# Optimization experiments

Measured on AMD Instinct MI355X. Metric: run time of the kernel, lower is better.

Reference implementation:

```python
import jax, jax.numpy as jnp
import numpy as np

DT = 0.042


def setup_inputs() -> dict:
    key = jax.random.key(0)
    ks = jax.random.split(key, 6)
    B, L, I, H = 64, 1024, 128, 512
    x = jax.random.normal(ks[0], (B, L, I), dtype=jnp.float32)
    x2h = jax.random.uniform(ks[1], (I, H), dtype=jnp.float32)  # rand * input_scaling (=1.0)
    h2h = jax.random.normal(ks[2], (H, H), dtype=jnp.float32) * (0.99 / (H ** 0.5))  # spectral-norm scaled
    bias = jax.random.uniform(ks[3], (H,), dtype=jnp.float32) * 2.0 - 1.0
    gamma = jax.random.uniform(ks[4], (H,), dtype=jnp.float32) + 2.0   # in [2, 3)
    epsilon = jax.random.uniform(ks[5], (H,), dtype=jnp.float32) + 4.0  # in [4, 5)
    return {"x": x, "x2h": x2h, "h2h": h2h, "bias": bias, "gamma": gamma, "epsilon": epsilon}


def reference(x, x2h, h2h, bias, gamma, epsilon):
    # x: (B, L, I). Precompute input projection for all timesteps in one GEMM.
    B, L, I = x.shape
    H = h2h.shape[0]
    u = jnp.einsum('bli,ih->blh', x, x2h) + bias  # (B, L, H)

    def step(carry, u_t):
        hy, hz = carry
        hz = hz + DT * (jnp.tanh(u_t + hy @ h2h) - gamma * hy - epsilon * hz)
        hy = hy + DT * hz
        return (hy, hz), hy

    init = (jnp.zeros((B, H), dtype=x.dtype), jnp.zeros((B, H), dtype=x.dtype))
    (hy_final, _), ys = jax.lax.scan(step, init, jnp.swapaxes(u, 0, 1))  # ys: (L, B, H)
    all_states = jnp.swapaxes(ys, 0, 1)  # (B, L, H)
    return all_states, hy_final
```

## Files before the change

### kernel.cpp

```cpp
#include <hip/hip_runtime.h>

#define DT 0.042f
constexpr int B = 64, L = 1024, I = 128, H = 512;

constexpr int NG = 32;
constexpr int NS = 8;
constexpr int GB = B / NG;
constexpr int SC = H / NS;

__global__ __launch_bounds__(256) void k_ugemm(const float* __restrict__ x,
                                               const float* __restrict__ w,
                                               const float* __restrict__ bias,
                                               float* __restrict__ u) {
    __shared__ __align__(16) float a_s[64][132];
    __shared__ __align__(16) float b_s[128][68];
    const int tx = threadIdx.x & 15;
    const int ty = threadIdx.x >> 4;
    const int row0 = blockIdx.x * 64;
    const int col0 = blockIdx.y * 64;

    for (int i = threadIdx.x; i < 64 * 32; i += 256) {
        int r = i >> 5, c4 = (i & 31) << 2;
        *(float4*)&a_s[r][c4] = *(const float4*)(x + (size_t)(row0 + r) * I + c4);
    }
    for (int i = threadIdx.x; i < 128 * 16; i += 256) {
        int k = i >> 4, c4 = (i & 15) << 2;
        *(float4*)&b_s[k][c4] = *(const float4*)(w + (size_t)k * H + col0 + c4);
    }
    __syncthreads();

    float acc[4][4] = {};
    for (int k = 0; k < I; k += 4) {
        float a4[4][4], b4[4][4];
        #pragma unroll
        for (int i = 0; i < 4; ++i) *(float4*)a4[i] = *(const float4*)&a_s[ty * 4 + i][k];
        #pragma unroll
        for (int kk = 0; kk < 4; ++kk) *(float4*)b4[kk] = *(const float4*)&b_s[k + kk][tx * 4];
        #pragma unroll
        for (int i = 0; i < 4; ++i)
            #pragma unroll
            for (int kk = 0; kk < 4; ++kk)
                #pragma unroll
                for (int j = 0; j < 4; ++j)
                    acc[i][j] += a4[i][kk] * b4[kk][j];
    }
    float4 bv = *(const float4*)&bias[col0 + tx * 4];
    #pragma unroll
    for (int i = 0; i < 4; ++i) {
        size_t r = (size_t)(row0 + ty * 4 + i);
        float4 o;
        o.x = acc[i][0] + bv.x; o.y = acc[i][1] + bv.y;
        o.z = acc[i][2] + bv.z; o.w = acc[i][3] + bv.w;
        *(float4*)&u[r * H + col0 + tx * 4] = o;
    }
}

__global__ __launch_bounds__(512, 2) void k_scan(float* __restrict__ su,
                                              const float* __restrict__ h2h,
                                              const float* __restrict__ gamma,
                                              const float* __restrict__ epsv,
                                              unsigned long long* __restrict__ wsq,
                                              float* __restrict__ hyfin) {
    __shared__ __align__(16) float hy_s[GB * H];
    __shared__ __align__(16) float red[NS * GB * SC];
    const int tid = threadIdx.x;
    const int g = blockIdx.x & 31;
    const int s = blockIdx.x >> 5;
    const int b0 = g * GB, c0 = s * SC;

    const int cc = tid & 63, kc = tid >> 6;
    const int scc = tid & 63, sb = (tid >> 6) & 1;
    const int sc_ = c0 + scc;

    float hreg[64];
    {
        const float* hp = h2h + (size_t)(kc * 64) * H + c0 + cc;
        #pragma unroll
        for (int kk = 0; kk < 64; ++kk) hreg[kk] = hp[(size_t)kk * H];
        #pragma unroll
        for (int kk = 0; kk < 64; ++kk) asm volatile("" : "+v"(hreg[kk]));
    }

    float gam = 0.f, ep = 0.f;
    float* su_p = nullptr;
    if (tid < 128) {
        gam = gamma[sc_]; ep = epsv[sc_];
        su_p = su + (size_t)(b0 + sb) * L * H + sc_;
    }
    unsigned long long* pollA = wsq + (size_t)b0 * H + (size_t)tid * 2;
    unsigned long long* pollB = pollA + (size_t)B * H;
    unsigned long long* dstA  = wsq + (size_t)(b0 + sb) * H + sc_;
    unsigned long long* dstB  = dstA + (size_t)B * H;

    float hy = 0.f, hz = 0.f;
    __syncthreads();

    for (int t = 0; t < L; ++t) {
        float uval = 0.f;
        if (tid < 128) uval = *su_p;

        if (t > 0) {
            unsigned long long* src = (t & 1) ? pollB : pollA;
            unsigned long long w0 = __hip_atomic_load(src + 0, __ATOMIC_RELAXED,
                                                      __HIP_MEMORY_SCOPE_AGENT);
            unsigned long long w1 = __hip_atomic_load(src + 1, __ATOMIC_RELAXED,
                                                      __HIP_MEMORY_SCOPE_AGENT);
            const unsigned tg = (unsigned)t;
            while ((unsigned)(w0 >> 32) != tg || (unsigned)(w1 >> 32) != tg) {
                if ((unsigned)(w0 >> 32) != tg)
                    w0 = __hip_atomic_load(src + 0, __ATOMIC_RELAXED,
                                           __HIP_MEMORY_SCOPE_AGENT);
                if ((unsigned)(w1 >> 32) != tg)
                    w1 = __hip_atomic_load(src + 1, __ATOMIC_RELAXED,
                                           __HIP_MEMORY_SCOPE_AGENT);
            }
            float2 hv;
            hv.x = __uint_as_float((unsigned)w0);
            hv.y = __uint_as_float((unsigned)w1);
            *(float2*)&hy_s[tid * 2] = hv;
        } else {
            *(float2*)&hy_s[tid * 2] = float2{0.f, 0.f};
        }
        __syncthreads();

        float acc0 = 0.f, acc1 = 0.f;
        const int k0 = kc * 64;
        #pragma unroll
        for (int q = 0; q < 16; ++q) {
            const float4 y0 = *(const float4*)&hy_s[0 * H + k0 + q * 4];
            const float4 y1 = *(const float4*)&hy_s[1 * H + k0 + q * 4];
            acc0 += hreg[q * 4 + 0] * y0.x + hreg[q * 4 + 1] * y0.y
                  + hreg[q * 4 + 2] * y0.z + hreg[q * 4 + 3] * y0.w;
            acc1 += hreg[q * 4 + 0] * y1.x + hreg[q * 4 + 1] * y1.y
                  + hreg[q * 4 + 2] * y1.z + hreg[q * 4 + 3] * y1.w;
        }
        red[kc * (GB * SC) + 0 * SC + cc] = acc0;
        red[kc * (GB * SC) + 1 * SC + cc] = acc1;
        __syncthreads();

        if (tid < 128) {
            const float* rq = red + sb * SC + scc;
            float m0 = rq[0 * 128] + rq[1 * 128];
            float m1 = rq[2 * 128] + rq[3 * 128];
            float m2 = rq[4 * 128] + rq[5 * 128];
            float m3 = rq[6 * 128] + rq[7 * 128];
            const float xx = uval + ((m0 + m1) + (m2 + m3));
            const float cx = fminf(fmaxf(xx, -10.f), 10.f);
            const float e2 = __expf(2.f * cx);
            const float th = (e2 - 1.f) / (e2 + 1.f);
            hz += DT * (th - gam * hy - ep * hz);
            hy += DT * hz;
            const unsigned long long wq =
                ((unsigned long long)(unsigned)(t + 1) << 32) | __float_as_uint(hy);
            __hip_atomic_store(((t + 1) & 1) ? dstB : dstA, wq,
                               __ATOMIC_RELAXED, __HIP_MEMORY_SCOPE_AGENT);
            *su_p = hy;
            su_p += H;
            if (t == L - 1) hyfin[(size_t)(b0 + sb) * H + sc_] = hy;
        }
        __syncthreads();
    }
}

extern "C" void kernel_launch(void* const* d_in, const int* in_sizes, int n_in,
                              void* d_out, int out_size, void* d_ws, size_t ws_size,
                              hipStream_t stream) {
    const float* x     = (const float*)d_in[0];
    const float* x2h   = (const float*)d_in[1];
    const float* h2h   = (const float*)d_in[2];
    const float* bias  = (const float*)d_in[3];
    const float* gamma = (const float*)d_in[4];
    const float* epsv  = (const float*)d_in[5];
    float* states = (float*)d_out;
    float* hyfin  = states + (size_t)B * L * H;

    unsigned long long* wsq = (unsigned long long*)d_ws;

    hipMemsetAsync(d_ws, 0, 2ull * B * H * 8, stream);
    dim3 g1(B * L / 64, H / 64);
    k_ugemm<<<g1, 256, 0, stream>>>(x, x2h, bias, states);
    k_scan<<<NG * NS, 512, 0, stream>>>(states, h2h, gamma, epsv, wsq, hyfin);
}
```

Measured before the change: 1.861 ms.

## Broadcast polled hidden state via wave readlane instead of shared memory

Each wavefront now polls exactly the 64 hidden values it needs for its K-chunk: lanes 0-31 take batch row 0 and lanes 32-63 take batch row 1. The values are then broadcast to all lanes with readlane instead of being staged through shared memory. This removes the shared hy buffer and one block-wide barrier per timestep, cutting per-step latency in this latency-bound recurrent scan. In exchange each wave polls global memory independently, readlane adds scalar work, and the asm register pin on hreg is removed.

```diff
diff --git a/kernel.cpp b/kernel.cpp
--- a/kernel.cpp
+++ b/kernel.cpp
@@ -61,14 +61,14 @@
                                               const float* __restrict__ epsv,
                                               unsigned long long* __restrict__ wsq,
                                               float* __restrict__ hyfin) {
-    __shared__ __align__(16) float hy_s[GB * H];
     __shared__ __align__(16) float red[NS * GB * SC];
     const int tid = threadIdx.x;
     const int g = blockIdx.x & 31;
     const int s = blockIdx.x >> 5;
     const int b0 = g * GB, c0 = s * SC;
 
-    const int cc = tid & 63, kc = tid >> 6;
+    const int cc = tid & 63;
+    const int kc = tid >> 6;
     const int scc = tid & 63, sb = (tid >> 6) & 1;
     const int sc_ = c0 + scc;
 
@@ -77,8 +77,6 @@
         const float* hp = h2h + (size_t)(kc * 64) * H + c0 + cc;
         #pragma unroll
         for (int kk = 0; kk < 64; ++kk) hreg[kk] = hp[(size_t)kk * H];
-        #pragma unroll
-        for (int kk = 0; kk < 64; ++kk) asm volatile("" : "+v"(hreg[kk]));
     }
 
     float gam = 0.f, ep = 0.f;
@@ -87,7 +85,8 @@
         gam = gamma[sc_]; ep = epsv[sc_];
         su_p = su + (size_t)(b0 + sb) * L * H + sc_;
     }
-    unsigned long long* pollA = wsq + (size_t)b0 * H + (size_t)tid * 2;
+    unsigned long long* pollA = wsq + (size_t)(b0 + (cc >> 5)) * H
+                                + kc * 64 + 2 * (cc & 31);
     unsigned long long* pollB = pollA + (size_t)B * H;
     unsigned long long* dstA  = wsq + (size_t)(b0 + sb) * H + sc_;
     unsigned long long* dstB  = dstA + (size_t)B * H;
@@ -99,6 +98,7 @@
         float uval = 0.f;
         if (tid < 128) uval = *su_p;
 
+        int hxi, hyi;
         if (t > 0) {
             unsigned long long* src = (t & 1) ? pollB : pollA;
             unsigned long long w0 = __hip_atomic_load(src + 0, __ATOMIC_RELAXED,
@@ -114,25 +114,21 @@
                     w1 = __hip_atomic_load(src + 1, __ATOMIC_RELAXED,
                                            __HIP_MEMORY_SCOPE_AGENT);
             }
-            float2 hv;
-            hv.x = __uint_as_float((unsigned)w0);
-            hv.y = __uint_as_float((unsigned)w1);
-            *(float2*)&hy_s[tid * 2] = hv;
+            hxi = (int)(unsigned)w0;
+            hyi = (int)(unsigned)w1;
         } else {
-            *(float2*)&hy_s[tid * 2] = float2{0.f, 0.f};
+            hxi = 0; hyi = 0;
         }
-        __syncthreads();
 
         float acc0 = 0.f, acc1 = 0.f;
-        const int k0 = kc * 64;
         #pragma unroll
-        for (int q = 0; q < 16; ++q) {
-            const float4 y0 = *(const float4*)&hy_s[0 * H + k0 + q * 4];
-            const float4 y1 = *(const float4*)&hy_s[1 * H + k0 + q * 4];
-            acc0 += hreg[q * 4 + 0] * y0.x + hreg[q * 4 + 1] * y0.y
-                  + hreg[q * 4 + 2] * y0.z + hreg[q * 4 + 3] * y0.w;
-            acc1 += hreg[q * 4 + 0] * y1.x + hreg[q * 4 + 1] * y1.y
-                  + hreg[q * 4 + 2] * y1.z + hreg[q * 4 + 3] * y1.w;
+        for (int j = 0; j < 32; ++j) {
+            const float a0 = __int_as_float(__builtin_amdgcn_readlane(hxi, j));
+            const float a1 = __int_as_float(__builtin_amdgcn_readlane(hyi, j));
+            const float b0f = __int_as_float(__builtin_amdgcn_readlane(hxi, 32 + j));
+            const float b1f = __int_as_float(__builtin_amdgcn_readlane(hyi, 32 + j));
+            acc0 += a0 * hreg[2 * j] + a1 * hreg[2 * j + 1];
+            acc1 += b0f * hreg[2 * j] + b1f * hreg[2 * j + 1];
         }
         red[kc * (GB * SC) + 0 * SC + cc] = acc0;
         red[kc * (GB * SC) + 1 * SC + cc] = acc1;
```

Result: slower. 2.277 ms (+22.3%).

## Make hy staging wave-local and double-buffer reduction to drop per-step barriers

Applied to the files above, without the earlier changes.

Each wavefront now polls only the slice of the previous hidden state that its own matvec chunk needs, and stores it into a private shared-memory slot. This removes the block-wide barrier between polling and the matvec. The partial-sum reduction buffer is double-buffered by timestep parity, which removes the trailing barrier, leaving one barrier per step in the serial recurrence. The change relies on same-wave ordering of shared-memory writes and reads, and it also drops the asm register-pinning of the h2h weights.

```diff
diff --git a/kernel.cpp b/kernel.cpp
--- a/kernel.cpp
+++ b/kernel.cpp
@@ -61,24 +61,23 @@
                                               const float* __restrict__ epsv,
                                               unsigned long long* __restrict__ wsq,
                                               float* __restrict__ hyfin) {
-    __shared__ __align__(16) float hy_s[GB * H];
-    __shared__ __align__(16) float red[NS * GB * SC];
+    __shared__ __align__(16) float hy_s[NS][GB][SC];
+    __shared__ __align__(16) float red[2][NS * GB * SC];
     const int tid = threadIdx.x;
     const int g = blockIdx.x & 31;
     const int s = blockIdx.x >> 5;
     const int b0 = g * GB, c0 = s * SC;
 
-    const int cc = tid & 63, kc = tid >> 6;
+    const int cc = tid & 63, w = tid >> 6;
+    const int pb = cc >> 5, pk = cc & 31;
     const int scc = tid & 63, sb = (tid >> 6) & 1;
     const int sc_ = c0 + scc;
 
     float hreg[64];
     {
-        const float* hp = h2h + (size_t)(kc * 64) * H + c0 + cc;
+        const float* hp = h2h + (size_t)(w * 64) * H + c0 + cc;
         #pragma unroll
         for (int kk = 0; kk < 64; ++kk) hreg[kk] = hp[(size_t)kk * H];
-        #pragma unroll
-        for (int kk = 0; kk < 64; ++kk) asm volatile("" : "+v"(hreg[kk]));
     }
 
     float gam = 0.f, ep = 0.f;
@@ -87,7 +86,7 @@
         gam = gamma[sc_]; ep = epsv[sc_];
         su_p = su + (size_t)(b0 + sb) * L * H + sc_;
     }
-    unsigned long long* pollA = wsq + (size_t)b0 * H + (size_t)tid * 2;
+    unsigned long long* pollA = wsq + (size_t)(b0 + pb) * H + w * 64 + 2 * pk;
     unsigned long long* pollB = pollA + (size_t)B * H;
     unsigned long long* dstA  = wsq + (size_t)(b0 + sb) * H + sc_;
     unsigned long long* dstB  = dstA + (size_t)B * H;
@@ -117,29 +116,32 @@
             float2 hv;
             hv.x = __uint_as_float((unsigned)w0);
             hv.y = __uint_as_float((unsigned)w1);
-            *(float2*)&hy_s[tid * 2] = hv;
+            *(float2*)&hy_s[w][pb][2 * pk] = hv;
         } else {
-            *(float2*)&hy_s[tid * 2] = float2{0.f, 0.f};
+            *(float2*)&hy_s[w][pb][2 * pk] = float2{0.f, 0.f};
         }
-        __syncthreads();
 
         float acc0 = 0.f, acc1 = 0.f;
-        const int k0 = kc * 64;
-        #pragma unroll
-        for (int q = 0; q < 16; ++q) {
-            const float4 y0 = *(const float4*)&hy_s[0 * H + k0 + q * 4];
-            const float4 y1 = *(const float4*)&hy_s[1 * H + k0 + q * 4];
-            acc0 += hreg[q * 4 + 0] * y0.x + hreg[q * 4 + 1] * y0.y
-                  + hreg[q * 4 + 2] * y0.z + hreg[q * 4 + 3] * y0.w;
-            acc1 += hreg[q * 4 + 0] * y1.x + hreg[q * 4 + 1] * y1.y
-                  + hreg[q * 4 + 2] * y1.z + hreg[q * 4 + 3] * y1.w;
+        {
+            const float* y0p = &hy_s[w][0][0];
+            const float* y1p = &hy_s[w][1][0];
+            #pragma unroll
+            for (int q = 0; q < 16; ++q) {
+                const float4 y0 = *(const float4*)(y0p + q * 4);
+                const float4 y1 = *(const float4*)(y1p + q * 4);
+                acc0 += hreg[q*4+0]*y0.x + hreg[q*4+1]*y0.y
+                      + hreg[q*4+2]*y0.z + hreg[q*4+3]*y0.w;
+                acc1 += hreg[q*4+0]*y1.x + hreg[q*4+1]*y1.y
+                      + hreg[q*4+2]*y1.z + hreg[q*4+3]*y1.w;
+            }
         }
-        red[kc * (GB * SC) + 0 * SC + cc] = acc0;
-        red[kc * (GB * SC) + 1 * SC + cc] = acc1;
+        float* rp = red[t & 1];
+        rp[w * (GB * SC) + 0 * SC + cc] = acc0;
+        rp[w * (GB * SC) + 1 * SC + cc] = acc1;
         __syncthreads();
 
         if (tid < 128) {
-            const float* rq = red + sb * SC + scc;
+            const float* rq = red[t & 1] + sb * SC + scc;
             float m0 = rq[0 * 128] + rq[1 * 128];
             float m1 = rq[2 * 128] + rq[3 * 128];
             float m2 = rq[4 * 128] + rq[5 * 128];
@@ -158,7 +160,6 @@
             su_p += H;
             if (t == L - 1) hyfin[(size_t)(b0 + sb) * H + sc_] = hy;
         }
-        __syncthreads();
     }
 }
 
```

Result: slower. 2.086 ms (+12.1%).

## Double-buffer reduction scratch, drop trailing barrier, poll with one wide load

Applied to the files above, without the earlier changes.

Double-buffers the shared reduction array by timestep parity so the block barrier at the end of each step can be removed. The two separate 64-bit atomic polls are replaced with a single 128-bit global load using sc1 cache bypass in inline asm. It also removes the asm register pinning of the h2h weights. The goal is to cut one barrier and one memory round trip from the serial per-timestep critical path. The risks are that a wide non-atomic load may see the two halves torn across updates, and that the compiler may spill the weight registers without the pinning.

```diff
diff --git a/kernel.cpp b/kernel.cpp
--- a/kernel.cpp
+++ b/kernel.cpp
@@ -62,7 +62,7 @@
                                               unsigned long long* __restrict__ wsq,
                                               float* __restrict__ hyfin) {
     __shared__ __align__(16) float hy_s[GB * H];
-    __shared__ __align__(16) float red[NS * GB * SC];
+    __shared__ __align__(16) float red[2][NS * GB * SC];
     const int tid = threadIdx.x;
     const int g = blockIdx.x & 31;
     const int s = blockIdx.x >> 5;
@@ -77,8 +77,6 @@
         const float* hp = h2h + (size_t)(kc * 64) * H + c0 + cc;
         #pragma unroll
         for (int kk = 0; kk < 64; ++kk) hreg[kk] = hp[(size_t)kk * H];
-        #pragma unroll
-        for (int kk = 0; kk < 64; ++kk) asm volatile("" : "+v"(hreg[kk]));
     }
 
     float gam = 0.f, ep = 0.f;
@@ -101,22 +99,19 @@
 
         if (t > 0) {
             unsigned long long* src = (t & 1) ? pollB : pollA;
-            unsigned long long w0 = __hip_atomic_load(src + 0, __ATOMIC_RELAXED,
-                                                      __HIP_MEMORY_SCOPE_AGENT);
-            unsigned long long w1 = __hip_atomic_load(src + 1, __ATOMIC_RELAXED,
-                                                      __HIP_MEMORY_SCOPE_AGENT);
             const unsigned tg = (unsigned)t;
-            while ((unsigned)(w0 >> 32) != tg || (unsigned)(w1 >> 32) != tg) {
-                if ((unsigned)(w0 >> 32) != tg)
-                    w0 = __hip_atomic_load(src + 0, __ATOMIC_RELAXED,
-                                           __HIP_MEMORY_SCOPE_AGENT);
-                if ((unsigned)(w1 >> 32) != tg)
-                    w1 = __hip_atomic_load(src + 1, __ATOMIC_RELAXED,
-                                           __HIP_MEMORY_SCOPE_AGENT);
+            ulonglong2 pw;
+            asm volatile("global_load_dwordx4 %0, %1, off sc1\n\t"
+                         "s_waitcnt vmcnt(0)"
+                         : "=v"(pw) : "v"(src) : "memory");
+            while ((unsigned)(pw.x >> 32) != tg || (unsigned)(pw.y >> 32) != tg) {
+                asm volatile("global_load_dwordx4 %0, %1, off sc1\n\t"
+                             "s_waitcnt vmcnt(0)"
+                             : "=v"(pw) : "v"(src) : "memory");
             }
             float2 hv;
-            hv.x = __uint_as_float((unsigned)w0);
-            hv.y = __uint_as_float((unsigned)w1);
+            hv.x = __uint_as_float((unsigned)pw.x);
+            hv.y = __uint_as_float((unsigned)pw.y);
             *(float2*)&hy_s[tid * 2] = hv;
         } else {
             *(float2*)&hy_s[tid * 2] = float2{0.f, 0.f};
@@ -134,12 +129,13 @@
             acc1 += hreg[q * 4 + 0] * y1.x + hreg[q * 4 + 1] * y1.y
                   + hreg[q * 4 + 2] * y1.z + hreg[q * 4 + 3] * y1.w;
         }
-        red[kc * (GB * SC) + 0 * SC + cc] = acc0;
-        red[kc * (GB * SC) + 1 * SC + cc] = acc1;
+        float* rp = red[t & 1];
+        rp[kc * (GB * SC) + 0 * SC + cc] = acc0;
+        rp[kc * (GB * SC) + 1 * SC + cc] = acc1;
         __syncthreads();
 
         if (tid < 128) {
-            const float* rq = red + sb * SC + scc;
+            const float* rq = red[t & 1] + sb * SC + scc;
             float m0 = rq[0 * 128] + rq[1 * 128];
             float m1 = rq[2 * 128] + rq[3 * 128];
             float m2 = rq[4 * 128] + rq[5 * 128];
@@ -158,7 +154,6 @@
             su_p += H;
             if (t == L - 1) hyfin[(size_t)(b0 + sb) * H + sc_] = hy;
         }
-        __syncthreads();
     }
 }
 
```

Measured after the change: 1.885 ms. No clear change (+1.3%).
